# Optimization experiments

Hardware: AMD Instinct MI355X
Metric: run time of the kernel (lower is better)

## Reference

```python
import jax, jax.numpy as jnp
import numpy as np
import math

D_MODEL = 768
N_HEADS = 12
HEAD_DIM = D_MODEL // N_HEADS
B, T = 2, 4096


def setup_inputs() -> dict:
    key = jax.random.key(0)
    k1, k2, k3, k4 = jax.random.split(key, 4)
    x = jax.random.normal(k1, (B, T, D_MODEL), dtype=jnp.float32)
    mask = jax.random.randint(k2, (B, T), 0, 2).astype(jnp.bool_)
    # torch Linear init scale ~ 1/sqrt(fan_in); use scaled normal for stability
    w_qkv = jax.random.normal(k3, (3 * D_MODEL, D_MODEL), dtype=jnp.float32) / math.sqrt(D_MODEL)
    w_proj = jax.random.normal(k4, (D_MODEL, D_MODEL), dtype=jnp.float32) / math.sqrt(D_MODEL)
    b_proj = jnp.zeros((D_MODEL,), dtype=jnp.float32)
    return {"x": x, "mask": mask, "w_qkv": w_qkv, "w_proj": w_proj, "b_proj": b_proj}


def reference(x, mask, w_qkv, w_proj, b_proj):
    Bb, Tt, D = x.shape
    H, Hd = N_HEADS, HEAD_DIM
    scale = math.sqrt(Hd)
    # qkv projection (bias-free): (B,T,3D) -> (3,B,H,T,Hd)
    qkv = jnp.einsum('btd,ed->bte', x, w_qkv)
    qkv = qkv.reshape(Bb, Tt, 3, H, Hd).transpose(2, 0, 3, 1, 4)
    q, k, v = qkv[0], qkv[1], qkv[2]
    # full T x T scores (faithful to non-fused original)
    attn = jnp.einsum('bhqd,bhkd->bhqk', q, k) / scale
    attn = jnp.where(mask[:, None, None, :], -jnp.inf, attn)
    attn = jax.nn.softmax(attn, axis=-1)  # dropout p=0 -> identity
    out = jnp.einsum('bhqk,bhkd->bhqd', attn, v)
    out = out.transpose(0, 2, 1, 3).reshape(Bb, Tt, D)
    return jnp.einsum('btd,ed->bte', out, w_proj) + b_proj
```

## Files before the change

kernel.cpp:

```cpp
#include <hip/hip_runtime.h>

#define D_MODEL 768
#define N_HEADS 12
#define SEQ 4096
#define KVB 128

typedef __attribute__((ext_vector_type(4))) float f32x4;
typedef __attribute__((ext_vector_type(16))) float f32x16;
typedef __attribute__((ext_vector_type(8))) short bf16x8;
typedef __attribute__((ext_vector_type(4))) unsigned short u16x4;

typedef __attribute__((address_space(3))) void lds_void;
typedef __attribute__((address_space(1))) const void glb_void;

static __device__ __forceinline__ void gld_lds16(const void* g, void* l) {
    __builtin_amdgcn_global_load_lds((glb_void*)g, (lds_void*)l, 16, 0, 0);
}

static __device__ __forceinline__ unsigned short f32_bf16(float f) {
    union { float f; unsigned int u; } c; c.f = f;
    unsigned int u = c.u;
    u += 0x7FFFu + ((u >> 16) & 1u);
    return (unsigned short)(u >> 16);
}

static __device__ __forceinline__ unsigned int cvtpk(float lo, float hi) {
    unsigned int r;
    asm("v_cvt_pk_bf16_f32 %0, %1, %2" : "=v"(r) : "v"(lo), "v"(hi));
    return r;
}

__global__ void cvt_bf16(const float* __restrict__ in, unsigned short* __restrict__ out, int n) {
    int i = (blockIdx.x * blockDim.x + threadIdx.x) * 4;
    int stride = gridDim.x * blockDim.x * 4;
    for (; i < n; i += stride) {
        f32x4 v = *(const f32x4*)(in + i);
        u16x4 o;
        o[0] = f32_bf16(v[0]); o[1] = f32_bf16(v[1]);
        o[2] = f32_bf16(v[2]); o[3] = f32_bf16(v[3]);
        *(u16x4*)(out + i) = o;
    }
}

#define QSCL 0.18033688f

__global__ __launch_bounds__(256) void qkv_gemm(const unsigned short* __restrict__ A,
                                                const unsigned short* __restrict__ Bw,
                                                unsigned short* __restrict__ qb,
                                                unsigned short* __restrict__ kb,
                                                unsigned short* __restrict__ vb) {
    __shared__ __attribute__((aligned(16))) unsigned short lA[128*32];
    __shared__ __attribute__((aligned(16))) unsigned short lB[128*32];
    const int K = 768;
    int tid = threadIdx.x;
    int wave = tid >> 6, lane = tid & 63;
    int qr = (wave >> 1) * 64, qc = (wave & 1) * 64;
    int m0 = blockIdx.x * 128, n0 = blockIdx.y * 128;
    f32x4 acc[4][4] = {};
    const int sl = (((lane >> 4) ^ (lane & 3)) * 16);

    for (int kt = 0; kt < K; kt += 32) {
        __syncthreads();
        #pragma unroll
        for (int i = 0; i < 2; ++i) {
            int c = i*256 + tid;
            int row = c >> 2;
            int col = ((c & 3) ^ (row & 3)) * 8;
            char* dA = (char*)lA + (i*256 + wave*64)*16;
            char* dB = (char*)lB + (i*256 + wave*64)*16;
            gld_lds16(A  + (size_t)(m0 + row) * K + kt + col, dA);
            gld_lds16(Bw + (size_t)(n0 + row) * K + kt + col, dB);
        }
        __syncthreads();
        bf16x8 af[4], bfr[4];
        #pragma unroll
        for (int m = 0; m < 4; ++m)
            af[m] = *(bf16x8*)((char*)lA + (qr + m*16 + (lane & 15))*64 + sl);
        #pragma unroll
        for (int n = 0; n < 4; ++n)
            bfr[n] = *(bf16x8*)((char*)lB + (qc + n*16 + (lane & 15))*64 + sl);
        #pragma unroll
        for (int m = 0; m < 4; ++m)
            #pragma unroll
            for (int n = 0; n < 4; ++n)
                acc[m][n] = __builtin_amdgcn_mfma_f32_16x16x32_bf16(af[m], bfr[n], acc[m][n], 0, 0, 0);
    }
    #pragma unroll
    for (int n = 0; n < 4; ++n) {
        int colg = n0 + qc + n*16 + (lane & 15);
        int s = colg / 768;
        int rem = colg - s * 768;
        int h = rem >> 6, d = rem & 63;
        if (s == 2) {
            #pragma unroll
            for (int m = 0; m < 4; ++m) {
                int rowb = m0 + qr + m*16 + (lane >> 4)*4;
                int bb = rowb >> 12, t0 = rowb & 4095;
                int t0p = (t0 & ~12) | ((t0 & 4) << 1) | ((t0 & 8) >> 1);
                u16x4 pk;
                #pragma unroll
                for (int r = 0; r < 4; ++r) pk[r] = f32_bf16(acc[m][n][r]);
                *(u16x4*)(vb + ((size_t)((bb*12 + h)*64 + d))*4096 + t0p) = pk;
            }
        } else {
            unsigned short* dst = (s == 0) ? qb : kb;
            float scl = (s == 0) ? QSCL : 1.0f;
            #pragma unroll
            for (int m = 0; m < 4; ++m) {
                int rowb = m0 + qr + m*16 + (lane >> 4)*4;
                #pragma unroll
                for (int r = 0; r < 4; ++r) {
                    int row = rowb + r;
                    int bb = row >> 12, t = row & 4095;
                    dst[((size_t)((bb*12 + h)*4096 + t))*64 + d] = f32_bf16(acc[m][n][r] * scl);
                }
            }
        }
    }
}

__global__ __launch_bounds__(512, 4) void attn_kern(const unsigned short* __restrict__ qbuf,
                                                    const unsigned short* __restrict__ kbuf,
                                                    const unsigned short* __restrict__ vtbuf,
                                                    const int* __restrict__ mask,
                                                    unsigned short* __restrict__ ob) {
    __shared__ __attribute__((aligned(16))) char lds[2][32768];
    __shared__ float lds_l[4][32];

    const int tid = threadIdx.x, wave = tid >> 6, lane = tid & 63;
    const int l31 = lane & 31, hi2 = lane >> 5;
    const int lane16 = lane * 16;
    const int wq = wave & 3, wk = wave >> 2;

    int raw = blockIdx.x;
    int sb = (raw & 7) * 96 + (raw >> 3);
    int bh = sb >> 5, qi = sb & 31;
    int q0 = qi * 128;
    int b = bh / 12, h = bh - b*12;

    const unsigned short* Qb = qbuf + (size_t)bh * SEQ * 64;
    const unsigned short* Kb = kbuf + (size_t)bh * SEQ * 64;
    const unsigned short* Vt = vtbuf + (size_t)bh * 64 * SEQ;
    const int* mrow = mask + b * SEQ + wk*64 + l31;

    bf16x8 bq[4];
    #pragma unroll
    for (int ds = 0; ds < 4; ++ds)
        bq[ds] = *(const bf16x8*)(Qb + (size_t)(q0 + wq*32 + l31)*64 + ds*16 + hi2*8);
    __builtin_amdgcn_sched_barrier(0);

    union U4 { unsigned int w[4]; bf16x8 v; };
    U4 bext; bext.w[0] = (hi2 == 0) ? 0x3F80u : 0u; bext.w[1] = bext.w[2] = bext.w[3] = 0u;

    auto stage = [&](char* buf, int kv0) {
        #pragma unroll
        for (int i = 0; i < 4; ++i) {
            int fi = wave*4 + i;
            const unsigned short* gsrc;
            if (fi < 16) {
                int kt = fi >> 2, ds = fi & 3;
                gsrc = Kb + (size_t)(kv0 + kt*32 + l31)*64 + ds*16 + hi2*8;
            } else {
                int g = fi - 16, dt = g >> 3, ks = g & 7;
                gsrc = Vt + (size_t)(dt*32 + l31)*4096 + kv0 + ks*16 + hi2*8;
            }
            gld_lds16(gsrc, buf + fi*1024);
        }
    };

    f32x16 oacc0 = {}, oacc1 = {};
    float lr = 0.0f;

    char* bA = lds[0];
    char* bB = lds[1];

    stage(bA, 0);
    int mbl0 = mrow[0], mbh0 = mrow[32];
    asm volatile("s_waitcnt vmcnt(0)" ::: "memory");
    __builtin_amdgcn_sched_barrier(0);
    __builtin_amdgcn_s_barrier();
    __builtin_amdgcn_sched_barrier(0);

    const int NT = SEQ / KVB;
    for (int t = 0; t < NT; ++t) {
        int mbl1 = 0, mbh1 = 0;
        if (t + 1 < NT) {
            stage(bB, (t + 1) * KVB);
            mbl1 = mrow[(t + 1) * KVB];
            mbh1 = mrow[(t + 1) * KVB + 32];
        }
        const char* bufK = bA;
        const char* bufV = bA + 16384;
        const int kt0 = wk*2, kt1 = wk*2 + 1;

        U4 ab0, ab1;
        ab0.w[0] = (hi2 == 0) ? (mbl0 ? 0xC480u : 0xC18Au) : 0u;
        ab0.w[1] = ab0.w[2] = ab0.w[3] = 0u;
        ab1.w[0] = (hi2 == 0) ? (mbh0 ? 0xC480u : 0xC18Au) : 0u;
        ab1.w[1] = ab1.w[2] = ab1.w[3] = 0u;

        f32x16 s0 = {}, s1 = {};
        s0 = __builtin_amdgcn_mfma_f32_32x32x16_bf16(ab0.v, bext.v, s0, 0, 0, 0);
        s1 = __builtin_amdgcn_mfma_f32_32x32x16_bf16(ab1.v, bext.v, s1, 0, 0, 0);
        #pragma unroll
        for (int ds = 0; ds < 4; ++ds) {
            bf16x8 aK0 = *(const bf16x8*)(bufK + (kt0*4 + ds)*1024 + lane16);
            bf16x8 aK1 = *(const bf16x8*)(bufK + (kt1*4 + ds)*1024 + lane16);
            s0 = __builtin_amdgcn_mfma_f32_32x32x16_bf16(aK0, bq[ds], s0, 0, 0, 0);
            s1 = __builtin_amdgcn_mfma_f32_32x32x16_bf16(aK1, bq[ds], s1, 0, 0, 0);
        }

        {
            float rs = 0.0f;
            #pragma unroll
            for (int i = 0; i < 16; ++i) { s0[i] = __builtin_amdgcn_exp2f(s0[i]); rs += s0[i]; }
            rs += __shfl_xor(rs, 32);
            lr += rs;
            U4 p0, p1;
            p0.w[0] = cvtpk(s0[0], s0[1]);   p0.w[1] = cvtpk(s0[2], s0[3]);
            p0.w[2] = cvtpk(s0[4], s0[5]);   p0.w[3] = cvtpk(s0[6], s0[7]);
            p1.w[0] = cvtpk(s0[8], s0[9]);   p1.w[1] = cvtpk(s0[10], s0[11]);
            p1.w[2] = cvtpk(s0[12], s0[13]); p1.w[3] = cvtpk(s0[14], s0[15]);
            int ka = kt0*2, kb2 = kt0*2 + 1;
            bf16x8 v00 = *(const bf16x8*)(bufV + (0*8 + ka)*1024 + lane16);
            bf16x8 v10 = *(const bf16x8*)(bufV + (1*8 + ka)*1024 + lane16);
            bf16x8 v01 = *(const bf16x8*)(bufV + (0*8 + kb2)*1024 + lane16);
            bf16x8 v11 = *(const bf16x8*)(bufV + (1*8 + kb2)*1024 + lane16);
            oacc0 = __builtin_amdgcn_mfma_f32_32x32x16_bf16(p0.v, v00, oacc0, 0, 0, 0);
            oacc1 = __builtin_amdgcn_mfma_f32_32x32x16_bf16(p0.v, v10, oacc1, 0, 0, 0);
            oacc0 = __builtin_amdgcn_mfma_f32_32x32x16_bf16(p1.v, v01, oacc0, 0, 0, 0);
            oacc1 = __builtin_amdgcn_mfma_f32_32x32x16_bf16(p1.v, v11, oacc1, 0, 0, 0);
        }
        {
            float rs = 0.0f;
            #pragma unroll
            for (int i = 0; i < 16; ++i) { s1[i] = __builtin_amdgcn_exp2f(s1[i]); rs += s1[i]; }
            rs += __shfl_xor(rs, 32);
            lr += rs;
            U4 p0, p1;
            p0.w[0] = cvtpk(s1[0], s1[1]);   p0.w[1] = cvtpk(s1[2], s1[3]);
            p0.w[2] = cvtpk(s1[4], s1[5]);   p0.w[3] = cvtpk(s1[6], s1[7]);
            p1.w[0] = cvtpk(s1[8], s1[9]);   p1.w[1] = cvtpk(s1[10], s1[11]);
            p1.w[2] = cvtpk(s1[12], s1[13]); p1.w[3] = cvtpk(s1[14], s1[15]);
            int ka = kt1*2, kb2 = kt1*2 + 1;
            bf16x8 v00 = *(const bf16x8*)(bufV + (0*8 + ka)*1024 + lane16);
            bf16x8 v10 = *(const bf16x8*)(bufV + (1*8 + ka)*1024 + lane16);
            bf16x8 v01 = *(const bf16x8*)(bufV + (0*8 + kb2)*1024 + lane16);
            bf16x8 v11 = *(const bf16x8*)(bufV + (1*8 + kb2)*1024 + lane16);
            oacc0 = __builtin_amdgcn_mfma_f32_32x32x16_bf16(p0.v, v00, oacc0, 0, 0, 0);
            oacc1 = __builtin_amdgcn_mfma_f32_32x32x16_bf16(p0.v, v10, oacc1, 0, 0, 0);
            oacc0 = __builtin_amdgcn_mfma_f32_32x32x16_bf16(p1.v, v01, oacc0, 0, 0, 0);
            oacc1 = __builtin_amdgcn_mfma_f32_32x32x16_bf16(p1.v, v11, oacc1, 0, 0, 0);
        }

        asm volatile("s_waitcnt vmcnt(0)" ::: "memory");
        __builtin_amdgcn_sched_barrier(0);
        __builtin_amdgcn_s_barrier();
        __builtin_amdgcn_sched_barrier(0);

        char* tmp = bA; bA = bB; bB = tmp;
        mbl0 = mbl1; mbh0 = mbh1;
    }

    float* cbase = (float*)lds + wq * 2048;
    if (wk == 1) {
        #pragma unroll
        for (int i = 0; i < 16; ++i) {
            cbase[i*64 + lane]        = oacc0[i];
            cbase[(16 + i)*64 + lane] = oacc1[i];
        }
        if (lane < 32) lds_l[wq][lane] = lr;
    }
    __syncthreads();
    if (wk == 0 && lane < 32) lds_l[wq][lane] += lr;
    __syncthreads();
    if (wk == 0) {
        #pragma unroll
        for (int r = 0; r < 16; ++r) {
            int q = (r & 3) + 8*(r >> 2) + 4*hi2;
            float inv = 1.0f / lds_l[wq][q];
            int tg = q0 + wq*32 + q;
            size_t base = ((size_t)(b*SEQ + tg)) * D_MODEL + h*64 + l31;
            ob[base]      = f32_bf16((oacc0[r] + cbase[r*64 + lane])        * inv);
            ob[base + 32] = f32_bf16((oacc1[r] + cbase[(16 + r)*64 + lane]) * inv);
        }
    }
}

__global__ __launch_bounds__(256) void proj_gemm(const unsigned short* __restrict__ A,
                                                 const unsigned short* __restrict__ Bw,
                                                 const float* __restrict__ bias,
                                                 float* __restrict__ out) {
    __shared__ __attribute__((aligned(16))) unsigned short lA[128*32];
    __shared__ __attribute__((aligned(16))) unsigned short lB[128*32];
    const int K = 768;
    int tid = threadIdx.x;
    int wave = tid >> 6, lane = tid & 63;
    int qr = (wave >> 1) * 64, qc = (wave & 1) * 64;
    int m0 = blockIdx.x * 128, n0 = blockIdx.y * 128;
    f32x4 acc[4][4] = {};
    const int sl = (((lane >> 4) ^ (lane & 3)) * 16);

    for (int kt = 0; kt < K; kt += 32) {
        __syncthreads();
        #pragma unroll
        for (int i = 0; i < 2; ++i) {
            int c = i*256 + tid;
            int row = c >> 2;
            int col = ((c & 3) ^ (row & 3)) * 8;
            char* dA = (char*)lA + (i*256 + wave*64)*16;
            char* dB = (char*)lB + (i*256 + wave*64)*16;
            gld_lds16(A  + (size_t)(m0 + row) * K + kt + col, dA);
            gld_lds16(Bw + (size_t)(n0 + row) * K + kt + col, dB);
        }
        __syncthreads();
        bf16x8 af[4], bfr[4];
        #pragma unroll
        for (int m = 0; m < 4; ++m)
            af[m] = *(bf16x8*)((char*)lA + (qr + m*16 + (lane & 15))*64 + sl);
        #pragma unroll
        for (int n = 0; n < 4; ++n)
            bfr[n] = *(bf16x8*)((char*)lB + (qc + n*16 + (lane & 15))*64 + sl);
        #pragma unroll
        for (int m = 0; m < 4; ++m)
            #pragma unroll
            for (int n = 0; n < 4; ++n)
                acc[m][n] = __builtin_amdgcn_mfma_f32_16x16x32_bf16(af[m], bfr[n], acc[m][n], 0, 0, 0);
    }
    #pragma unroll
    for (int n = 0; n < 4; ++n) {
        int colg = n0 + qc + n*16 + (lane & 15);
        float bn = bias[colg];
        #pragma unroll
        for (int m = 0; m < 4; ++m) {
            int rowb = m0 + qr + m*16 + (lane >> 4)*4;
            #pragma unroll
            for (int r = 0; r < 4; ++r)
                out[(size_t)(rowb + r) * 768 + colg] = acc[m][n][r] + bn;
        }
    }
}

extern "C" void kernel_launch(void* const* d_in, const int* in_sizes, int n_in,
                              void* d_out, int out_size, void* d_ws, size_t ws_size,
                              hipStream_t stream) {
    const float* x      = (const float*)d_in[0];
    const int*   mask   = (const int*)d_in[1];
    const float* w_qkv  = (const float*)d_in[2];
    const float* w_proj = (const float*)d_in[3];
    const float* b_proj = (const float*)d_in[4];
    float* out = (float*)d_out;

    unsigned short* ws = (unsigned short*)d_ws;
    unsigned short* xb     = ws;
    unsigned short* wqkvb  = xb     + 6291456;
    unsigned short* wprojb = wqkvb  + 1769472;
    unsigned short* qb     = wprojb + 589824;
    unsigned short* kb     = qb     + 6291456;
    unsigned short* vtb    = kb     + 6291456;
    unsigned short* ob     = vtb    + 6291456;

    cvt_bf16<<<1024, 256, 0, stream>>>(x,      xb,     6291456);
    cvt_bf16<<<256,  256, 0, stream>>>(w_qkv,  wqkvb,  1769472);
    cvt_bf16<<<128,  256, 0, stream>>>(w_proj, wprojb, 589824);

    qkv_gemm<<<dim3(64, 18), 256, 0, stream>>>(xb, wqkvb, qb, kb, vtb);
    attn_kern<<<768, 512, 0, stream>>>(qb, kb, vtb, mask, ob);
    proj_gemm<<<dim3(64, 6), 256, 0, stream>>>(ob, wprojb, b_proj, out);
}
```

Baseline: 214.5 us.

## Load V fragments directly from global into registers instead of staging in LDS

The V tile is no longer copied into shared memory. Each wave now reads its V operand fragments straight from global memory into registers at the start of every KV step, and only K is staged. This halves the LDS footprint per block, which can let more blocks reside per CU, and removes the LDS reads for V. In exchange, the four waves sharing a key range each fetch the same V data separately, adding L2 traffic and exposing global latency before the PV MFMAs. The constant score offset for unmasked keys is also dropped to zero; it cancels in the final normalisation but removes headroom against exp2 overflow.

```diff
diff --git a/kernel.cpp b/kernel.cpp
--- a/kernel.cpp
+++ b/kernel.cpp
@@ -124,7 +124,7 @@
                                                     const unsigned short* __restrict__ vtbuf,
                                                     const int* __restrict__ mask,
                                                     unsigned short* __restrict__ ob) {
-    __shared__ __attribute__((aligned(16))) char lds[2][32768];
+    __shared__ __attribute__((aligned(16))) char lds[2][16384];
     __shared__ float lds_l[4][32];
 
     const int tid = threadIdx.x, wave = tid >> 6, lane = tid & 63;
@@ -154,19 +154,15 @@
 
     auto stage = [&](char* buf, int kv0) {
         #pragma unroll
-        for (int i = 0; i < 4; ++i) {
-            int fi = wave*4 + i;
-            const unsigned short* gsrc;
-            if (fi < 16) {
-                int kt = fi >> 2, ds = fi & 3;
-                gsrc = Kb + (size_t)(kv0 + kt*32 + l31)*64 + ds*16 + hi2*8;
-            } else {
-                int g = fi - 16, dt = g >> 3, ks = g & 7;
-                gsrc = Vt + (size_t)(dt*32 + l31)*4096 + kv0 + ks*16 + hi2*8;
-            }
-            gld_lds16(gsrc, buf + fi*1024);
+        for (int i = 0; i < 2; ++i) {
+            int fi = wave*2 + i;
+            int kt = fi >> 2, ds = fi & 3;
+            gld_lds16(Kb + (size_t)(kv0 + kt*32 + l31)*64 + ds*16 + hi2*8, buf + fi*1024);
         }
     };
+
+    const unsigned short* vp0 = Vt + (size_t)l31 * 4096 + wk*64 + hi2*8;
+    const unsigned short* vp1 = vp0 + (size_t)32 * 4096;
 
     f32x16 oacc0 = {}, oacc1 = {};
     float lr = 0.0f;
@@ -189,14 +185,23 @@
             mbl1 = mrow[(t + 1) * KVB];
             mbh1 = mrow[(t + 1) * KVB + 32];
         }
+
+        bf16x8 vA0 = *(const bf16x8*)(vp0 +  0);
+        bf16x8 vA1 = *(const bf16x8*)(vp0 + 16);
+        bf16x8 vA2 = *(const bf16x8*)(vp0 + 32);
+        bf16x8 vA3 = *(const bf16x8*)(vp0 + 48);
+        bf16x8 vB0 = *(const bf16x8*)(vp1 +  0);
+        bf16x8 vB1 = *(const bf16x8*)(vp1 + 16);
+        bf16x8 vB2 = *(const bf16x8*)(vp1 + 32);
+        bf16x8 vB3 = *(const bf16x8*)(vp1 + 48);
+
         const char* bufK = bA;
-        const char* bufV = bA + 16384;
         const int kt0 = wk*2, kt1 = wk*2 + 1;
 
         U4 ab0, ab1;
-        ab0.w[0] = (hi2 == 0) ? (mbl0 ? 0xC480u : 0xC18Au) : 0u;
+        ab0.w[0] = (hi2 == 0) ? (mbl0 ? 0xC480u : 0u) : 0u;
         ab0.w[1] = ab0.w[2] = ab0.w[3] = 0u;
-        ab1.w[0] = (hi2 == 0) ? (mbh0 ? 0xC480u : 0xC18Au) : 0u;
+        ab1.w[0] = (hi2 == 0) ? (mbh0 ? 0xC480u : 0u) : 0u;
         ab1.w[1] = ab1.w[2] = ab1.w[3] = 0u;
 
         f32x16 s0 = {}, s1 = {};
@@ -221,15 +226,10 @@
             p0.w[2] = cvtpk(s0[4], s0[5]);   p0.w[3] = cvtpk(s0[6], s0[7]);
             p1.w[0] = cvtpk(s0[8], s0[9]);   p1.w[1] = cvtpk(s0[10], s0[11]);
             p1.w[2] = cvtpk(s0[12], s0[13]); p1.w[3] = cvtpk(s0[14], s0[15]);
-            int ka = kt0*2, kb2 = kt0*2 + 1;
-            bf16x8 v00 = *(const bf16x8*)(bufV + (0*8 + ka)*1024 + lane16);
-            bf16x8 v10 = *(const bf16x8*)(bufV + (1*8 + ka)*1024 + lane16);
-            bf16x8 v01 = *(const bf16x8*)(bufV + (0*8 + kb2)*1024 + lane16);
-            bf16x8 v11 = *(const bf16x8*)(bufV + (1*8 + kb2)*1024 + lane16);
-            oacc0 = __builtin_amdgcn_mfma_f32_32x32x16_bf16(p0.v, v00, oacc0, 0, 0, 0);
-            oacc1 = __builtin_amdgcn_mfma_f32_32x32x16_bf16(p0.v, v10, oacc1, 0, 0, 0);
-            oacc0 = __builtin_amdgcn_mfma_f32_32x32x16_bf16(p1.v, v01, oacc0, 0, 0, 0);
-            oacc1 = __builtin_amdgcn_mfma_f32_32x32x16_bf16(p1.v, v11, oacc1, 0, 0, 0);
+            oacc0 = __builtin_amdgcn_mfma_f32_32x32x16_bf16(p0.v, vA0, oacc0, 0, 0, 0);
+            oacc1 = __builtin_amdgcn_mfma_f32_32x32x16_bf16(p0.v, vB0, oacc1, 0, 0, 0);
+            oacc0 = __builtin_amdgcn_mfma_f32_32x32x16_bf16(p1.v, vA1, oacc0, 0, 0, 0);
+            oacc1 = __builtin_amdgcn_mfma_f32_32x32x16_bf16(p1.v, vB1, oacc1, 0, 0, 0);
         }
         {
             float rs = 0.0f;
@@ -242,15 +242,10 @@
             p0.w[2] = cvtpk(s1[4], s1[5]);   p0.w[3] = cvtpk(s1[6], s1[7]);
             p1.w[0] = cvtpk(s1[8], s1[9]);   p1.w[1] = cvtpk(s1[10], s1[11]);
             p1.w[2] = cvtpk(s1[12], s1[13]); p1.w[3] = cvtpk(s1[14], s1[15]);
-            int ka = kt1*2, kb2 = kt1*2 + 1;
-            bf16x8 v00 = *(const bf16x8*)(bufV + (0*8 + ka)*1024 + lane16);
-            bf16x8 v10 = *(const bf16x8*)(bufV + (1*8 + ka)*1024 + lane16);
-            bf16x8 v01 = *(const bf16x8*)(bufV + (0*8 + kb2)*1024 + lane16);
-            bf16x8 v11 = *(const bf16x8*)(bufV + (1*8 + kb2)*1024 + lane16);
-            oacc0 = __builtin_amdgcn_mfma_f32_32x32x16_bf16(p0.v, v00, oacc0, 0, 0, 0);
-            oacc1 = __builtin_amdgcn_mfma_f32_32x32x16_bf16(p0.v, v10, oacc1, 0, 0, 0);
-            oacc0 = __builtin_amdgcn_mfma_f32_32x32x16_bf16(p1.v, v01, oacc0, 0, 0, 0);
-            oacc1 = __builtin_amdgcn_mfma_f32_32x32x16_bf16(p1.v, v11, oacc1, 0, 0, 0);
+            oacc0 = __builtin_amdgcn_mfma_f32_32x32x16_bf16(p0.v, vA2, oacc0, 0, 0, 0);
+            oacc1 = __builtin_amdgcn_mfma_f32_32x32x16_bf16(p0.v, vB2, oacc1, 0, 0, 0);
+            oacc0 = __builtin_amdgcn_mfma_f32_32x32x16_bf16(p1.v, vA3, oacc0, 0, 0, 0);
+            oacc1 = __builtin_amdgcn_mfma_f32_32x32x16_bf16(p1.v, vB3, oacc1, 0, 0, 0);
         }
 
         asm volatile("s_waitcnt vmcnt(0)" ::: "memory");
@@ -260,6 +255,7 @@
 
         char* tmp = bA; bA = bB; bB = tmp;
         mbl0 = mbl1; mbh0 = mbh1;
+        vp0 += KVB; vp1 += KVB;
     }
 
     float* cbase = (float*)lds + wq * 2048;
```

Result: slower. 326.4 us (+52.1%).

## Single-buffer V tile to cut LDS and raise attention occupancy

Applied to the files above, without the earlier changes.

Shrinks the attention kernel's LDS from two full K+V buffers to double-buffered K plus a single V buffer, and raises the launch-bounds occupancy hint from 4 to 6 blocks. V for the current tile is now loaded at the start of each iteration and waited on with a partial vmcnt plus an extra barrier before the PV matmuls, so the exp/convert work overlaps the V load. The unmasked score bias changes from a constant offset to zero. The added barrier per iteration and the V load exposed within the iteration may offset the occupancy gain, and the higher occupancy target may cause register spills.

```diff
diff --git a/kernel.cpp b/kernel.cpp
--- a/kernel.cpp
+++ b/kernel.cpp
@@ -119,12 +119,12 @@
     }
 }
 
-__global__ __launch_bounds__(512, 4) void attn_kern(const unsigned short* __restrict__ qbuf,
+__global__ __launch_bounds__(512, 6) void attn_kern(const unsigned short* __restrict__ qbuf,
                                                     const unsigned short* __restrict__ kbuf,
                                                     const unsigned short* __restrict__ vtbuf,
                                                     const int* __restrict__ mask,
                                                     unsigned short* __restrict__ ob) {
-    __shared__ __attribute__((aligned(16))) char lds[2][32768];
+    __shared__ __attribute__((aligned(16))) char lds[49152];
     __shared__ float lds_l[4][32];
 
     const int tid = threadIdx.x, wave = tid >> 6, lane = tid & 63;
@@ -152,29 +152,31 @@
     union U4 { unsigned int w[4]; bf16x8 v; };
     U4 bext; bext.w[0] = (hi2 == 0) ? 0x3F80u : 0u; bext.w[1] = bext.w[2] = bext.w[3] = 0u;
 
-    auto stage = [&](char* buf, int kv0) {
-        #pragma unroll
-        for (int i = 0; i < 4; ++i) {
-            int fi = wave*4 + i;
-            const unsigned short* gsrc;
-            if (fi < 16) {
-                int kt = fi >> 2, ds = fi & 3;
-                gsrc = Kb + (size_t)(kv0 + kt*32 + l31)*64 + ds*16 + hi2*8;
-            } else {
-                int g = fi - 16, dt = g >> 3, ks = g & 7;
-                gsrc = Vt + (size_t)(dt*32 + l31)*4096 + kv0 + ks*16 + hi2*8;
-            }
-            gld_lds16(gsrc, buf + fi*1024);
+    char* bK0 = lds;
+    char* bK1 = lds + 16384;
+    char* bufV = lds + 32768;
+
+    auto stageK = [&](char* buf, int kv0) {
+        #pragma unroll
+        for (int i = 0; i < 2; ++i) {
+            int fi = wave*2 + i;
+            int kt = fi >> 2, ds = fi & 3;
+            gld_lds16(Kb + (size_t)(kv0 + kt*32 + l31)*64 + ds*16 + hi2*8, buf + fi*1024);
+        }
+    };
+    auto stageV = [&](int kv0) {
+        #pragma unroll
+        for (int i = 0; i < 2; ++i) {
+            int g = wave*2 + i;
+            int dt = g >> 3, ks = g & 7;
+            gld_lds16(Vt + (size_t)(dt*32 + l31)*4096 + kv0 + ks*16 + hi2*8, bufV + g*1024);
         }
     };
 
     f32x16 oacc0 = {}, oacc1 = {};
     float lr = 0.0f;
 
-    char* bA = lds[0];
-    char* bB = lds[1];
-
-    stage(bA, 0);
+    stageK(bK0, 0);
     int mbl0 = mrow[0], mbh0 = mrow[32];
     asm volatile("s_waitcnt vmcnt(0)" ::: "memory");
     __builtin_amdgcn_sched_barrier(0);
@@ -183,20 +185,25 @@
 
     const int NT = SEQ / KVB;
     for (int t = 0; t < NT; ++t) {
+        int kv0 = t * KVB;
+        char* bufK  = (t & 1) ? bK1 : bK0;
+        char* bufKn = (t & 1) ? bK0 : bK1;
+
+        stageV(kv0);
+        __builtin_amdgcn_sched_barrier(0);
         int mbl1 = 0, mbh1 = 0;
         if (t + 1 < NT) {
-            stage(bB, (t + 1) * KVB);
-            mbl1 = mrow[(t + 1) * KVB];
-            mbh1 = mrow[(t + 1) * KVB + 32];
-        }
-        const char* bufK = bA;
-        const char* bufV = bA + 16384;
+            stageK(bufKn, kv0 + KVB);
+            mbl1 = mrow[kv0 + KVB];
+            mbh1 = mrow[kv0 + KVB + 32];
+        }
+
         const int kt0 = wk*2, kt1 = wk*2 + 1;
 
         U4 ab0, ab1;
-        ab0.w[0] = (hi2 == 0) ? (mbl0 ? 0xC480u : 0xC18Au) : 0u;
+        ab0.w[0] = (hi2 == 0) ? (mbl0 ? 0xC480u : 0u) : 0u;
         ab0.w[1] = ab0.w[2] = ab0.w[3] = 0u;
-        ab1.w[0] = (hi2 == 0) ? (mbh0 ? 0xC480u : 0xC18Au) : 0u;
+        ab1.w[0] = (hi2 == 0) ? (mbh0 ? 0xC480u : 0u) : 0u;
         ab1.w[1] = ab1.w[2] = ab1.w[3] = 0u;
 
         f32x16 s0 = {}, s1 = {};
@@ -210,47 +217,60 @@
             s1 = __builtin_amdgcn_mfma_f32_32x32x16_bf16(aK1, bq[ds], s1, 0, 0, 0);
         }
 
+        U4 p0A, p1A, p0B, p1B;
         {
             float rs = 0.0f;
             #pragma unroll
             for (int i = 0; i < 16; ++i) { s0[i] = __builtin_amdgcn_exp2f(s0[i]); rs += s0[i]; }
             rs += __shfl_xor(rs, 32);
             lr += rs;
-            U4 p0, p1;
-            p0.w[0] = cvtpk(s0[0], s0[1]);   p0.w[1] = cvtpk(s0[2], s0[3]);
-            p0.w[2] = cvtpk(s0[4], s0[5]);   p0.w[3] = cvtpk(s0[6], s0[7]);
-            p1.w[0] = cvtpk(s0[8], s0[9]);   p1.w[1] = cvtpk(s0[10], s0[11]);
-            p1.w[2] = cvtpk(s0[12], s0[13]); p1.w[3] = cvtpk(s0[14], s0[15]);
+            p0A.w[0] = cvtpk(s0[0], s0[1]);   p0A.w[1] = cvtpk(s0[2], s0[3]);
+            p0A.w[2] = cvtpk(s0[4], s0[5]);   p0A.w[3] = cvtpk(s0[6], s0[7]);
+            p1A.w[0] = cvtpk(s0[8], s0[9]);   p1A.w[1] = cvtpk(s0[10], s0[11]);
+            p1A.w[2] = cvtpk(s0[12], s0[13]); p1A.w[3] = cvtpk(s0[14], s0[15]);
+        }
+        {
+            float rs = 0.0f;
+            #pragma unroll
+            for (int i = 0; i < 16; ++i) { s1[i] = __builtin_amdgcn_exp2f(s1[i]); rs += s1[i]; }
+            rs += __shfl_xor(rs, 32);
+            lr += rs;
+            p0B.w[0] = cvtpk(s1[0], s1[1]);   p0B.w[1] = cvtpk(s1[2], s1[3]);
+            p0B.w[2] = cvtpk(s1[4], s1[5]);   p0B.w[3] = cvtpk(s1[6], s1[7]);
+            p1B.w[0] = cvtpk(s1[8], s1[9]);   p1B.w[1] = cvtpk(s1[10], s1[11]);
+            p1B.w[2] = cvtpk(s1[12], s1[13]); p1B.w[3] = cvtpk(s1[14], s1[15]);
+        }
+
+        if (t + 1 < NT) {
+            asm volatile("s_waitcnt vmcnt(4)" ::: "memory");
+        } else {
+            asm volatile("s_waitcnt vmcnt(0)" ::: "memory");
+        }
+        __builtin_amdgcn_sched_barrier(0);
+        __builtin_amdgcn_s_barrier();
+        __builtin_amdgcn_sched_barrier(0);
+
+        {
             int ka = kt0*2, kb2 = kt0*2 + 1;
             bf16x8 v00 = *(const bf16x8*)(bufV + (0*8 + ka)*1024 + lane16);
             bf16x8 v10 = *(const bf16x8*)(bufV + (1*8 + ka)*1024 + lane16);
             bf16x8 v01 = *(const bf16x8*)(bufV + (0*8 + kb2)*1024 + lane16);
             bf16x8 v11 = *(const bf16x8*)(bufV + (1*8 + kb2)*1024 + lane16);
-            oacc0 = __builtin_amdgcn_mfma_f32_32x32x16_bf16(p0.v, v00, oacc0, 0, 0, 0);
-            oacc1 = __builtin_amdgcn_mfma_f32_32x32x16_bf16(p0.v, v10, oacc1, 0, 0, 0);
-            oacc0 = __builtin_amdgcn_mfma_f32_32x32x16_bf16(p1.v, v01, oacc0, 0, 0, 0);
-            oacc1 = __builtin_amdgcn_mfma_f32_32x32x16_bf16(p1.v, v11, oacc1, 0, 0, 0);
+            oacc0 = __builtin_amdgcn_mfma_f32_32x32x16_bf16(p0A.v, v00, oacc0, 0, 0, 0);
+            oacc1 = __builtin_amdgcn_mfma_f32_32x32x16_bf16(p0A.v, v10, oacc1, 0, 0, 0);
+            oacc0 = __builtin_amdgcn_mfma_f32_32x32x16_bf16(p1A.v, v01, oacc0, 0, 0, 0);
+            oacc1 = __builtin_amdgcn_mfma_f32_32x32x16_bf16(p1A.v, v11, oacc1, 0, 0, 0);
         }
         {
-            float rs = 0.0f;
-            #pragma unroll
-            for (int i = 0; i < 16; ++i) { s1[i] = __builtin_amdgcn_exp2f(s1[i]); rs += s1[i]; }
-            rs += __shfl_xor(rs, 32);
-            lr += rs;
-            U4 p0, p1;
-            p0.w[0] = cvtpk(s1[0], s1[1]);   p0.w[1] = cvtpk(s1[2], s1[3]);
-            p0.w[2] = cvtpk(s1[4], s1[5]);   p0.w[3] = cvtpk(s1[6], s1[7]);
-            p1.w[0] = cvtpk(s1[8], s1[9]);   p1.w[1] = cvtpk(s1[10], s1[11]);
-            p1.w[2] = cvtpk(s1[12], s1[13]); p1.w[3] = cvtpk(s1[14], s1[15]);
             int ka = kt1*2, kb2 = kt1*2 + 1;
             bf16x8 v00 = *(const bf16x8*)(bufV + (0*8 + ka)*1024 + lane16);
             bf16x8 v10 = *(const bf16x8*)(bufV + (1*8 + ka)*1024 + lane16);
             bf16x8 v01 = *(const bf16x8*)(bufV + (0*8 + kb2)*1024 + lane16);
             bf16x8 v11 = *(const bf16x8*)(bufV + (1*8 + kb2)*1024 + lane16);
-            oacc0 = __builtin_amdgcn_mfma_f32_32x32x16_bf16(p0.v, v00, oacc0, 0, 0, 0);
-            oacc1 = __builtin_amdgcn_mfma_f32_32x32x16_bf16(p0.v, v10, oacc1, 0, 0, 0);
-            oacc0 = __builtin_amdgcn_mfma_f32_32x32x16_bf16(p1.v, v01, oacc0, 0, 0, 0);
-            oacc1 = __builtin_amdgcn_mfma_f32_32x32x16_bf16(p1.v, v11, oacc1, 0, 0, 0);
+            oacc0 = __builtin_amdgcn_mfma_f32_32x32x16_bf16(p0B.v, v00, oacc0, 0, 0, 0);
+            oacc1 = __builtin_amdgcn_mfma_f32_32x32x16_bf16(p0B.v, v10, oacc1, 0, 0, 0);
+            oacc0 = __builtin_amdgcn_mfma_f32_32x32x16_bf16(p1B.v, v01, oacc0, 0, 0, 0);
+            oacc1 = __builtin_amdgcn_mfma_f32_32x32x16_bf16(p1B.v, v11, oacc1, 0, 0, 0);
         }
 
         asm volatile("s_waitcnt vmcnt(0)" ::: "memory");
@@ -258,7 +278,6 @@
         __builtin_amdgcn_s_barrier();
         __builtin_amdgcn_sched_barrier(0);
 
-        char* tmp = bA; bA = bB; bB = tmp;
         mbl0 = mbl1; mbh0 = mbh1;
     }
 
```

Result: slower. 466.4 us (+117.4%).
